# Kernel optimization log

Hardware: AMD Instinct MI355X
Metric: run time of the kernel (lower is better)

The kernel has to match this reference:

```python
import jax, jax.numpy as jnp
import numpy as np


def gcn_conv(x, src, dst, W, b, n_nodes):
    # PyG GCNConv default: add self-loops, symmetric normalization D^-1/2 A D^-1/2.
    h = x @ W  # [N, out]
    # degree with unit edge weights + self loop
    deg = jnp.zeros((n_nodes,), dtype=x.dtype).at[dst].add(1.0) + 1.0
    dinv = jax.lax.rsqrt(deg)  # deg >= 1, safe
    norm = dinv[src] * dinv[dst]  # [E]
    msg = h[src] * norm[:, None]  # [E, out] gather + scale
    out = jnp.zeros_like(h).at[dst].add(msg)  # scatter-add aggregate
    # self-loop contribution: norm_ii = dinv_i^2
    out = out + h * (dinv * dinv)[:, None]
    return out + b


def setup_inputs() -> dict:
    key = jax.random.key(0)
    ks = jax.random.split(key, 10)
    N, E, F_in, H, G = 100000, 1600000, 128, 128, 256
    x = jax.random.normal(ks[0], (N, F_in), dtype=jnp.float32)
    edge_index = jax.random.randint(ks[1], (2, E), 0, N, dtype=jnp.int64)
    batch = jnp.sort(jax.random.randint(ks[2], (N,), 0, G, dtype=jnp.int64))
    s1 = 1.0 / np.sqrt(F_in)
    s2 = 1.0 / np.sqrt(H)
    W1 = jax.random.uniform(ks[3], (F_in, H), jnp.float32, -s1, s1)
    b1 = jnp.zeros((H,), jnp.float32)
    W2 = jax.random.uniform(ks[4], (H, H), jnp.float32, -s2, s2)
    b2 = jnp.zeros((H,), jnp.float32)
    Wlin = jax.random.uniform(ks[5], (H, 2), jnp.float32, -s2, s2)
    blin = jax.random.uniform(ks[6], (2,), jnp.float32, -s2, s2)
    return {"x": x, "edge_index": edge_index, "batch": batch, "num_graphs": G,
            "W1": W1, "b1": b1, "W2": W2, "b2": b2, "Wlin": Wlin, "blin": blin}


def reference(x, edge_index, batch, num_graphs, W1, b1, W2, b2, Wlin, blin):
    n_nodes = x.shape[0]
    src, dst = edge_index[0], edge_index[1]
    h = jax.nn.relu(gcn_conv(x, src, dst, W1, b1, n_nodes))
    h = jax.nn.relu(gcn_conv(h, src, dst, W2, b2, n_nodes))
    # global_mean_pool over graphs
    sums = jax.ops.segment_sum(h, batch, num_segments=num_graphs)
    counts = jax.ops.segment_sum(jnp.ones((n_nodes,), h.dtype), batch, num_segments=num_graphs)
    pooled = sums / jnp.maximum(counts, 1.0)[:, None]  # [G, H]
    return pooled @ Wlin + blin  # [G, 2]
```

## Files before the change

### kernel.cpp

```cpp
#include <hip/hip_runtime.h>
#include <hip/hip_bf16.h>


#define FEAT 128
#define GRAPHS 256
#define CH 2048
#define BSH 8
#define MAXNB 512

typedef short bf16x8 __attribute__((ext_vector_type(8)));
typedef float f32x4 __attribute__((ext_vector_type(4)));

__device__ inline unsigned bf16rne(float f) {
    unsigned u = __float_as_uint(f);
    return (u + 0x7FFFu + ((u >> 16) & 1u)) >> 16;
}

#define SWZ(row, kbyte) ((kbyte) ^ (((row) & 7) << 4))

__global__ __launch_bounds__(256) void kb_hist(const int* __restrict__ dst, int E, int NB,
                                               int* __restrict__ bhist) {
    __shared__ int h[MAXNB];
    for (int i = threadIdx.x; i < NB; i += 256) h[i] = 0;
    __syncthreads();
    int stride = gridDim.x * 256;
    for (int i = blockIdx.x * 256 + threadIdx.x; i < E; i += stride)
        atomicAdd(&h[dst[i] >> BSH], 1);
    __syncthreads();
    for (int i = threadIdx.x; i < NB; i += 256)
        if (h[i]) atomicAdd(&bhist[i], h[i]);
}

__global__ void kb_scan(const int* __restrict__ bhist, int NB,
                        int* __restrict__ bbase, int* __restrict__ bcur) {
    __shared__ int s[512];
    int t = threadIdx.x;
    int v = (t < NB) ? bhist[t] : 0;
    s[t] = v;
    __syncthreads();
    for (int d = 1; d < 512; d <<= 1) {
        int a = (t >= d) ? s[t - d] : 0;
        __syncthreads();
        s[t] += a;
        __syncthreads();
    }
    if (t < NB) { int e = s[t] - v; bbase[t] = e; bcur[t] = e; }
}

__global__ __launch_bounds__(256) void kb_group(const int* __restrict__ src,
                                                const int* __restrict__ dst, int E, int NB,
                                                int* __restrict__ bcur,
                                                unsigned* __restrict__ stg) {
    __shared__ int lhist[MAXNB], lcur[MAXNB], gdelta[MAXNB], sc[512];
    __shared__ unsigned lpak[CH];
    __shared__ int gp[CH];
    int t = threadIdx.x;
    int base = blockIdx.x * CH;
    int n = E - base; if (n > CH) n = CH;

    for (int i = t; i < NB; i += 256) lhist[i] = 0;
    __syncthreads();

    unsigned pk[8]; int bk[8]; int nl = 0;
#pragma unroll
    for (int j = 0; j < 8; ++j) {
        int k = j * 256 + t;
        if (k < n) {
            int d = dst[base + k];
            int sv = src[base + k];
            int b = d >> BSH;
            pk[nl] = ((unsigned)(d & ((1 << BSH) - 1)) << 17) | (unsigned)sv;
            bk[nl] = b; nl++;
            atomicAdd(&lhist[b], 1);
        }
    }
    __syncthreads();

    for (int i = t; i < 512; i += 256) sc[i] = (i < NB) ? lhist[i] : 0;
    __syncthreads();
    for (int d = 1; d < 512; d <<= 1) {
        int a0 = (t >= d) ? sc[t - d] : 0;
        int a1 = sc[t + 256 - d];
        __syncthreads();
        sc[t] += a0; sc[t + 256] += a1;
        __syncthreads();
    }
    for (int i = t; i < NB; i += 256) {
        int c = lhist[i];
        int lb = sc[i] - c;
        lcur[i] = lb;
        int g = c ? atomicAdd(&bcur[i], c) : 0;
        gdelta[i] = g - lb;
    }
    __syncthreads();

    for (int j = 0; j < nl; ++j) {
        int b = bk[j];
        int slot = atomicAdd(&lcur[b], 1);
        lpak[slot] = pk[j];
        gp[slot] = gdelta[b] + slot;
    }
    __syncthreads();
    for (int i = t; i < n; i += 256) stg[gp[i]] = lpak[i];
}

__global__ __launch_bounds__(256) void kb_csr(const unsigned* __restrict__ stg,
                                              const int* __restrict__ bbase,
                                              const int* __restrict__ bhist, int N,
                                              int* __restrict__ ssrc, int* __restrict__ off,
                                              int* __restrict__ cnt, float* __restrict__ dinv) {
    __shared__ int h[256], lcur[256], sc[256];
    int b = blockIdx.x;
    int t = threadIdx.x;
    int s0 = bbase[b], m = bhist[b];
    h[t] = 0;
    __syncthreads();
    for (int i = t; i < m; i += 256) atomicAdd(&h[stg[s0 + i] >> 17], 1);
    __syncthreads();
    int v = h[t];
    sc[t] = v;
    __syncthreads();
    for (int d = 1; d < 256; d <<= 1) {
        int a = (t >= d) ? sc[t - d] : 0;
        __syncthreads();
        sc[t] += a;
        __syncthreads();
    }
    int lb = sc[t] - v;
    lcur[t] = lb;
    int node = (b << BSH) + t;
    if (node < N) {
        off[node] = s0 + lb;
        cnt[node] = v;
        dinv[node] = rsqrtf(1.0f + (float)v);
    }
    __syncthreads();
    for (int i = t; i < m; i += 256) {
        unsigned p = stg[s0 + i];
        int d = p >> 17;
        int r = atomicAdd(&lcur[d], 1);
        ssrc[s0 + r] = (int)(p & 0x1FFFFu);
    }
}

__global__ void k_gstart(const int* __restrict__ batch, int N, int G, int* __restrict__ gstart) {
    int i = blockIdx.x * blockDim.x + threadIdx.x;
    if (i >= N) return;
    int b = batch[i];
    int bp = (i == 0) ? -1 : batch[i - 1];
    for (int g = bp + 1; g <= b; ++g) gstart[g] = i;
    if (i == N - 1) {
        for (int g = b + 1; g <= G; ++g) gstart[g] = N;
    }
}

__global__ void k_wpre(const float* __restrict__ W, unsigned short* __restrict__ Wpre) {
    int tid = blockIdx.x * 256 + threadIdx.x;
    int frag = tid >> 6;
    int l = tid & 63;
    int cf = frag >> 2, ks = frag & 3;
    int col = cf * 16 + (l & 15);
    int k0 = ks * 32 + (l >> 4) * 8;
    unsigned short o[8];
#pragma unroll
    for (int j = 0; j < 8; ++j)
        o[j] = (unsigned short)bf16rne(W[(k0 + j) * 128 + col]);
    *(uint4*)(Wpre + (size_t)tid * 8) = *(const uint4*)o;
}

template <bool BF16IN>
__global__ __launch_bounds__(256, 4) void k_gemm_mfma(const void* __restrict__ Xv,
                                                      const unsigned short* __restrict__ Wpre,
                                                      const float* __restrict__ dinv,
                                                      unsigned short* __restrict__ HSB, int N) {
    __shared__ __align__(16) unsigned short sA[128 * 128];
    int t = threadIdx.x;
    int r0 = blockIdx.x * 128;
    int rows = N - r0; if (rows > 128) rows = 128;

    if constexpr (!BF16IN) {
        const float4* X4 = (const float4*)((const float*)Xv + (size_t)r0 * 128);
#pragma unroll
        for (int j = 0; j < 16; ++j) {
            int f = j * 256 + t;
            int row = f >> 5, q = f & 31;
            float4 v = make_float4(0.f, 0.f, 0.f, 0.f);
            if (row < rows) v = X4[f];
            unsigned lo = bf16rne(v.x) | (bf16rne(v.y) << 16);
            unsigned hi = bf16rne(v.z) | (bf16rne(v.w) << 16);
            int byte = row * 256 + SWZ(row, q * 8);
            *(uint2*)((char*)sA + byte) = make_uint2(lo, hi);
        }
    } else {
        const uint4* X4 = (const uint4*)((const unsigned short*)Xv + (size_t)r0 * 128);
#pragma unroll
        for (int j = 0; j < 8; ++j) {
            int f = j * 256 + t;
            int row = f >> 4, q = f & 15;
            uint4 v = make_uint4(0u, 0u, 0u, 0u);
            if (row < rows) v = X4[f];
            int byte = row * 256 + SWZ(row, q * 16);
            *(uint4*)((char*)sA + byte) = v;
        }
    }
    __syncthreads();

    int w = t >> 6, l = t & 63;
    int wr = (w >> 1) * 64, wc = (w & 1) * 64;
    int lr = l & 15, kc = l >> 4;

    f32x4 acc[4][4] = {};
    for (int ks = 0; ks < 4; ++ks) {
        bf16x8 a[4], b[4];
#pragma unroll
        for (int m = 0; m < 4; ++m) {
            int row = wr + m * 16 + lr;
            int byte = row * 256 + SWZ(row, ks * 64 + kc * 16);
            a[m] = *(const bf16x8*)((const char*)sA + byte);
        }
#pragma unroll
        for (int n = 0; n < 4; ++n) {
            int cf = (wc >> 4) + n;
            b[n] = *(const bf16x8*)(Wpre + ((size_t)((cf * 4 + ks) * 64 + l) * 8));
        }
#pragma unroll
        for (int m = 0; m < 4; ++m)
#pragma unroll
            for (int n = 0; n < 4; ++n)
                acc[m][n] = __builtin_amdgcn_mfma_f32_16x16x32_bf16(a[m], b[n], acc[m][n], 0, 0, 0);
    }
    __syncthreads();

#pragma unroll
    for (int m = 0; m < 4; ++m) {
        int rbase = wr + m * 16 + kc * 4;
#pragma unroll
        for (int r = 0; r < 4; ++r) {
            int row = rbase + r;
            float dv = (r0 + row < N) ? dinv[r0 + row] : 0.f;
#pragma unroll
            for (int n = 0; n < 4; ++n) {
                int col = wc + n * 16 + lr;
                sA[row * 128 + col] = (unsigned short)bf16rne(acc[m][n][r] * dv);
            }
        }
    }
    __syncthreads();
    uint4* dst4 = (uint4*)(HSB + (size_t)r0 * 128);
    const uint4* s4 = (const uint4*)sA;
#pragma unroll
    for (int j = 0; j < 8; ++j) {
        int f = j * 256 + t;
        int row = f >> 4;
        if (row < rows) dst4[f] = s4[f];
    }
}

#define GATHER1(uu)  { acc.x += __uint_as_float((uu) << 16); acc.y += __uint_as_float((uu) & 0xFFFF0000u); }
__global__ __launch_bounds__(256) void k_agg(const unsigned short* __restrict__ HSB,
                                             const int* __restrict__ off,
                                             const int* __restrict__ cnt,
                                             const int* __restrict__ ssrc,
                                             const float* __restrict__ dinv,
                                             const float* __restrict__ b,
                                             unsigned* __restrict__ OUTB, int N) {
    int wid = (blockIdx.x * blockDim.x + threadIdx.x) >> 6;
    int l = threadIdx.x & 63;
    if (wid >= N) return;
    int v = wid;
    const unsigned* T = (const unsigned*)HSB;
    unsigned su = T[(size_t)v * 64 + l];
    float2 acc;
    acc.x = __uint_as_float(su << 16);
    acc.y = __uint_as_float(su & 0xFFFF0000u);
    int s = off[v], e = s + cnt[v];
    int i = s;
    int head = (4 - (s & 3)) & 3;
    if (head > e - s) head = e - s;
    for (int k = 0; k < head; ++k, ++i) {
        unsigned u = T[(size_t)ssrc[i] * 64 + l];
        GATHER1(u)
    }
    for (; i + 8 <= e; i += 8) {
        int4 sa = *(const int4*)(ssrc + i);
        int4 sb = *(const int4*)(ssrc + i + 4);
        unsigned u0 = T[(size_t)sa.x * 64 + l];
        unsigned u1 = T[(size_t)sa.y * 64 + l];
        unsigned u2 = T[(size_t)sa.z * 64 + l];
        unsigned u3 = T[(size_t)sa.w * 64 + l];
        unsigned u4 = T[(size_t)sb.x * 64 + l];
        unsigned u5 = T[(size_t)sb.y * 64 + l];
        unsigned u6 = T[(size_t)sb.z * 64 + l];
        unsigned u7 = T[(size_t)sb.w * 64 + l];
        GATHER1(u0) GATHER1(u1) GATHER1(u2) GATHER1(u3)
        GATHER1(u4) GATHER1(u5) GATHER1(u6) GATHER1(u7)
    }
    if (i + 4 <= e) {
        int4 sa = *(const int4*)(ssrc + i);
        unsigned u0 = T[(size_t)sa.x * 64 + l];
        unsigned u1 = T[(size_t)sa.y * 64 + l];
        unsigned u2 = T[(size_t)sa.z * 64 + l];
        unsigned u3 = T[(size_t)sa.w * 64 + l];
        GATHER1(u0) GATHER1(u1) GATHER1(u2) GATHER1(u3)
        i += 4;
    }
    for (; i < e; ++i) {
        unsigned u = T[(size_t)ssrc[i] * 64 + l];
        GATHER1(u)
    }
    float dv = dinv[v];
    float2 bb = ((const float2*)b)[l];
    float ox = fmaxf(acc.x * dv + bb.x, 0.0f);
    float oy = fmaxf(acc.y * dv + bb.y, 0.0f);
    OUTB[(size_t)v * 64 + l] = bf16rne(ox) | (bf16rne(oy) << 16);
}

__global__ __launch_bounds__(256) void k_pool_head(const unsigned* __restrict__ H2,
                                                   const int* __restrict__ gstart,
                                                   const float* __restrict__ Wlin,
                                                   const float* __restrict__ blin,
                                                   float* __restrict__ out, int G) {
    __shared__ float2 stmp[256];
    __shared__ float sp[128];
    int g = blockIdx.x;
    int t = threadIdx.x;
    int p = t & 63, quarter = t >> 6;
    int s = gstart[g], e = gstart[g + 1];
    float2 acc = make_float2(0.f, 0.f);
    for (int i = s + quarter; i < e; i += 4) {
        unsigned u = H2[(size_t)i * 64 + p];
        acc.x += __uint_as_float(u << 16);
        acc.y += __uint_as_float(u & 0xFFFF0000u);
    }
    stmp[t] = acc;
    __syncthreads();
    if (t < 64) {
        float2 a = stmp[t];
        a.x += stmp[t + 64].x + stmp[t + 128].x + stmp[t + 192].x;
        a.y += stmp[t + 64].y + stmp[t + 128].y + stmp[t + 192].y;
        float inv = 1.0f / fmaxf((float)(e - s), 1.0f);
        sp[2 * t] = a.x * inv;
        sp[2 * t + 1] = a.y * inv;
    }
    __syncthreads();
    if (t < 2) {
        float a = 0.0f;
        for (int j = 0; j < 128; ++j) a += sp[j] * Wlin[j * 2 + t];
        out[g * 2 + t] = a + blin[t];
    }
}

extern "C" void kernel_launch(void* const* d_in, const int* in_sizes, int n_in,
                              void* d_out, int out_size, void* d_ws, size_t ws_size,
                              hipStream_t stream) {
    const float* x     = (const float*)d_in[0];
    const int*   ei    = (const int*)d_in[1];
    const int*   batch = (const int*)d_in[2];
    const float* W1    = (const float*)d_in[4];
    const float* b1    = (const float*)d_in[5];
    const float* W2    = (const float*)d_in[6];
    const float* b2    = (const float*)d_in[7];
    const float* Wlin  = (const float*)d_in[8];
    const float* blin  = (const float*)d_in[9];
    float* out = (float*)d_out;

    const int N = in_sizes[0] / FEAT;
    const int E = in_sizes[1] / 2;
    const int G = GRAPHS;
    const int NB = (N + (1 << BSH) - 1) >> BSH;
    const int* src = ei;
    const int* dst = ei + E;

    char* ws = (char*)d_ws;
    unsigned short* hsb = (unsigned short*)ws;
    unsigned short* hact = hsb + (size_t)N * FEAT;
    int*   ssrc = (int*)(hact + (size_t)N * FEAT);
    unsigned* stg = (unsigned*)(ssrc + E);
    int*   off  = (int*)(stg + E);
    int*   cnt  = off + N;
    float* dinv = (float*)(cnt + N);
    int*   bhist = (int*)(dinv + N);
    int*   bbase = bhist + MAXNB;
    int*   bcur  = bbase + MAXNB;
    int*   gstart = bcur + MAXNB;
    unsigned short* wpre1 = (unsigned short*)(gstart + G + 2);
    unsigned short* wpre2 = wpre1 + 16384;

    const int nb = (N + 255) / 256;
    const int nch = (E + CH - 1) / CH;
    const int ngb = (N + 127) / 128;

    hipMemsetAsync(bhist, 0, (size_t)NB * sizeof(int), stream);

    k_wpre<<<8, 256, 0, stream>>>(W1, wpre1);
    k_wpre<<<8, 256, 0, stream>>>(W2, wpre2);

    kb_hist<<<256, 256, 0, stream>>>(dst, E, NB, bhist);
    kb_scan<<<1, 512, 0, stream>>>(bhist, NB, bbase, bcur);
    kb_group<<<nch, 256, 0, stream>>>(src, dst, E, NB, bcur, stg);
    kb_csr<<<NB, 256, 0, stream>>>(stg, bbase, bhist, N, ssrc, off, cnt, dinv);

    k_gstart<<<nb, 256, 0, stream>>>(batch, N, G, gstart);

    k_gemm_mfma<false><<<ngb, 256, 0, stream>>>(x, wpre1, dinv, hsb, N);
    k_agg<<<(N + 3) / 4, 256, 0, stream>>>(hsb, off, cnt, ssrc, dinv, b1, (unsigned*)hact, N);
    k_gemm_mfma<true><<<ngb, 256, 0, stream>>>(hact, wpre2, dinv, hsb, N);
    k_agg<<<(N + 3) / 4, 256, 0, stream>>>(hsb, off, cnt, ssrc, dinv, b2, (unsigned*)hact, N);

    k_pool_head<<<G, 256, 0, stream>>>((const unsigned*)hact, gstart, Wlin, blin, out, G);
}
```

Measured before the change: 377.5 us.

## Quantize GEMM output to per-row int8 and gather int8 in aggregation

The GEMM epilogue now computes a per-row absmax scale and writes the scaled features as offset-by-128 int8 with a float scale per row, instead of bf16. The aggregation kernel gathers 4 bytes per lane, splits each node's edge list between two half-waves, dequantizes using the row scales, and combines the halves with a shuffle. This halves the bytes of the gather-bound aggregation, in exchange for int8 quantization error beyond the bf16 path and extra scale loads per edge.

```diff
diff --git a/kernel.cpp b/kernel.cpp
--- a/kernel.cpp
+++ b/kernel.cpp
@@ -168,12 +168,31 @@
     *(uint4*)(Wpre + (size_t)tid * 8) = *(const uint4*)o;
 }
 
+__device__ inline unsigned umax16pair(unsigned d, unsigned cur) {
+    unsigned a = d & 0x7FFF7FFFu;
+    unsigned lo = a & 0xFFFFu, hi = a >> 16;
+    unsigned m = lo > hi ? lo : hi;
+    return m > cur ? m : cur;
+}
+__device__ inline unsigned q8b(float x, float si) {
+    return (unsigned)(__float2int_rn(x * si) + 128) & 0xFFu;
+}
+__device__ inline unsigned pack2(unsigned d0, unsigned d1, float si) {
+    float x0 = __uint_as_float(d0 << 16);
+    float x1 = __uint_as_float(d0 & 0xFFFF0000u);
+    float x2 = __uint_as_float(d1 << 16);
+    float x3 = __uint_as_float(d1 & 0xFFFF0000u);
+    return q8b(x0, si) | (q8b(x1, si) << 8) | (q8b(x2, si) << 16) | (q8b(x3, si) << 24);
+}
+
 template <bool BF16IN>
 __global__ __launch_bounds__(256, 4) void k_gemm_mfma(const void* __restrict__ Xv,
                                                       const unsigned short* __restrict__ Wpre,
                                                       const float* __restrict__ dinv,
-                                                      unsigned short* __restrict__ HSB, int N) {
+                                                      unsigned char* __restrict__ Q8,
+                                                      float* __restrict__ srow, int N) {
     __shared__ __align__(16) unsigned short sA[128 * 128];
+    __shared__ unsigned sMaxH[256];
     int t = threadIdx.x;
     int r0 = blockIdx.x * 128;
     int rows = N - r0; if (rows > 128) rows = 128;
@@ -246,73 +265,115 @@
         }
     }
     __syncthreads();
-    uint4* dst4 = (uint4*)(HSB + (size_t)r0 * 128);
-    const uint4* s4 = (const uint4*)sA;
-#pragma unroll
-    for (int j = 0; j < 8; ++j) {
-        int f = j * 256 + t;
-        int row = f >> 4;
-        if (row < rows) dst4[f] = s4[f];
-    }
-}
-
-#define GATHER1(uu)  { acc.x += __uint_as_float((uu) << 16); acc.y += __uint_as_float((uu) & 0xFFFF0000u); }
-__global__ __launch_bounds__(256) void k_agg(const unsigned short* __restrict__ HSB,
-                                             const int* __restrict__ off,
-                                             const int* __restrict__ cnt,
-                                             const int* __restrict__ ssrc,
-                                             const float* __restrict__ dinv,
-                                             const float* __restrict__ b,
-                                             unsigned* __restrict__ OUTB, int N) {
+
+    {
+        int r = t >> 1, hh = t & 1;
+        const uint4* rowp = (const uint4*)(sA + r * 128 + hh * 64);
+        uint4 wreg[8];
+#pragma unroll
+        for (int j = 0; j < 8; ++j) wreg[j] = rowp[j];
+        unsigned mb = 0;
+#pragma unroll
+        for (int j = 0; j < 8; ++j) {
+            mb = umax16pair(wreg[j].x, mb);
+            mb = umax16pair(wreg[j].y, mb);
+            mb = umax16pair(wreg[j].z, mb);
+            mb = umax16pair(wreg[j].w, mb);
+        }
+        sMaxH[r * 2 + hh] = mb;
+        __syncthreads();
+        unsigned m0 = sMaxH[r * 2], m1 = sMaxH[r * 2 + 1];
+        unsigned m16 = m0 > m1 ? m0 : m1;
+        float mv = __uint_as_float(m16 << 16);
+        float si = (mv > 0.f) ? 127.0f / mv : 0.0f;
+        if (hh == 0 && r0 + r < N) srow[r0 + r] = mv * (1.0f / 127.0f);
+        if (r0 + r < N) {
+            unsigned q[16];
+#pragma unroll
+            for (int j = 0; j < 8; ++j) {
+                q[2 * j]     = pack2(wreg[j].x, wreg[j].y, si);
+                q[2 * j + 1] = pack2(wreg[j].z, wreg[j].w, si);
+            }
+            uint4* qo = (uint4*)(Q8 + (size_t)(r0 + r) * 128 + hh * 64);
+            qo[0] = make_uint4(q[0], q[1], q[2], q[3]);
+            qo[1] = make_uint4(q[4], q[5], q[6], q[7]);
+            qo[2] = make_uint4(q[8], q[9], q[10], q[11]);
+            qo[3] = make_uint4(q[12], q[13], q[14], q[15]);
+        }
+    }
+}
+
+#define ACC8(d, sc) { float _s = (sc);                       \
+    a0 += _s * (float)((d) & 0xFFu);                         \
+    a1 += _s * (float)(((d) >> 8) & 0xFFu);                  \
+    a2 += _s * (float)(((d) >> 16) & 0xFFu);                 \
+    a3 += _s * (float)((d) >> 24);                           \
+    ssum += _s; }
+
+__global__ __launch_bounds__(256) void k_agg8(const unsigned char* __restrict__ Q8,
+                                              const float* __restrict__ srow,
+                                              const int* __restrict__ off,
+                                              const int* __restrict__ cnt,
+                                              const int* __restrict__ ssrc,
+                                              const float* __restrict__ dinv,
+                                              const float* __restrict__ b,
+                                              unsigned* __restrict__ OUTB, int N) {
     int wid = (blockIdx.x * blockDim.x + threadIdx.x) >> 6;
+    if (wid >= N) return;
     int l = threadIdx.x & 63;
-    if (wid >= N) return;
+    int half = l >> 5, c4 = l & 31;
     int v = wid;
-    const unsigned* T = (const unsigned*)HSB;
-    unsigned su = T[(size_t)v * 64 + l];
-    float2 acc;
-    acc.x = __uint_as_float(su << 16);
-    acc.y = __uint_as_float(su & 0xFFFF0000u);
-    int s = off[v], e = s + cnt[v];
-    int i = s;
-    int head = (4 - (s & 3)) & 3;
-    if (head > e - s) head = e - s;
-    for (int k = 0; k < head; ++k, ++i) {
-        unsigned u = T[(size_t)ssrc[i] * 64 + l];
-        GATHER1(u)
-    }
-    for (; i + 8 <= e; i += 8) {
-        int4 sa = *(const int4*)(ssrc + i);
-        int4 sb = *(const int4*)(ssrc + i + 4);
-        unsigned u0 = T[(size_t)sa.x * 64 + l];
-        unsigned u1 = T[(size_t)sa.y * 64 + l];
-        unsigned u2 = T[(size_t)sa.z * 64 + l];
-        unsigned u3 = T[(size_t)sa.w * 64 + l];
-        unsigned u4 = T[(size_t)sb.x * 64 + l];
-        unsigned u5 = T[(size_t)sb.y * 64 + l];
-        unsigned u6 = T[(size_t)sb.z * 64 + l];
-        unsigned u7 = T[(size_t)sb.w * 64 + l];
-        GATHER1(u0) GATHER1(u1) GATHER1(u2) GATHER1(u3)
-        GATHER1(u4) GATHER1(u5) GATHER1(u6) GATHER1(u7)
-    }
-    if (i + 4 <= e) {
-        int4 sa = *(const int4*)(ssrc + i);
-        unsigned u0 = T[(size_t)sa.x * 64 + l];
-        unsigned u1 = T[(size_t)sa.y * 64 + l];
-        unsigned u2 = T[(size_t)sa.z * 64 + l];
-        unsigned u3 = T[(size_t)sa.w * 64 + l];
-        GATHER1(u0) GATHER1(u1) GATHER1(u2) GATHER1(u3)
-        i += 4;
-    }
-    for (; i < e; ++i) {
-        unsigned u = T[(size_t)ssrc[i] * 64 + l];
-        GATHER1(u)
-    }
-    float dv = dinv[v];
-    float2 bb = ((const float2*)b)[l];
-    float ox = fmaxf(acc.x * dv + bb.x, 0.0f);
-    float oy = fmaxf(acc.y * dv + bb.y, 0.0f);
-    OUTB[(size_t)v * 64 + l] = bf16rne(ox) | (bf16rne(oy) << 16);
+    int s = off[v], c = cnt[v];
+    int K = (c + 1) >> 1;
+    int ib = s + (half ? K : 0);
+    int ie = half ? (s + c) : (s + K);
+
+    float a0 = 0.f, a1 = 0.f, a2 = 0.f, a3 = 0.f, ssum = 0.f;
+    if (!half) {
+        unsigned d = *(const unsigned*)(Q8 + (size_t)v * 128 + c4 * 4);
+        float sc = srow[v];
+        ACC8(d, sc)
+    }
+    while (ib + 8 <= ie) {
+        int u0 = ssrc[ib],     u1 = ssrc[ib + 1], u2 = ssrc[ib + 2], u3 = ssrc[ib + 3];
+        int u4 = ssrc[ib + 4], u5 = ssrc[ib + 5], u6 = ssrc[ib + 6], u7 = ssrc[ib + 7];
+        unsigned d0 = *(const unsigned*)(Q8 + (size_t)u0 * 128 + c4 * 4);
+        unsigned d1 = *(const unsigned*)(Q8 + (size_t)u1 * 128 + c4 * 4);
+        unsigned d2 = *(const unsigned*)(Q8 + (size_t)u2 * 128 + c4 * 4);
+        unsigned d3 = *(const unsigned*)(Q8 + (size_t)u3 * 128 + c4 * 4);
+        unsigned d4 = *(const unsigned*)(Q8 + (size_t)u4 * 128 + c4 * 4);
+        unsigned d5 = *(const unsigned*)(Q8 + (size_t)u5 * 128 + c4 * 4);
+        unsigned d6 = *(const unsigned*)(Q8 + (size_t)u6 * 128 + c4 * 4);
+        unsigned d7 = *(const unsigned*)(Q8 + (size_t)u7 * 128 + c4 * 4);
+        float s0 = srow[u0], s1 = srow[u1], s2 = srow[u2], s3 = srow[u3];
+        float s4 = srow[u4], s5 = srow[u5], s6 = srow[u6], s7 = srow[u7];
+        ACC8(d0, s0) ACC8(d1, s1) ACC8(d2, s2) ACC8(d3, s3)
+        ACC8(d4, s4) ACC8(d5, s5) ACC8(d6, s6) ACC8(d7, s7)
+        ib += 8;
+    }
+    while (ib < ie) {
+        int u = ssrc[ib++];
+        unsigned d = *(const unsigned*)(Q8 + (size_t)u * 128 + c4 * 4);
+        float sc = srow[u];
+        ACC8(d, sc)
+    }
+    a0 += __shfl_xor(a0, 32);
+    a1 += __shfl_xor(a1, 32);
+    a2 += __shfl_xor(a2, 32);
+    a3 += __shfl_xor(a3, 32);
+    ssum += __shfl_xor(ssum, 32);
+    if (!half) {
+        float dv = dinv[v];
+        float4 bb = *(const float4*)(b + c4 * 4);
+        float o0 = fmaxf((a0 - 128.f * ssum) * dv + bb.x, 0.f);
+        float o1 = fmaxf((a1 - 128.f * ssum) * dv + bb.y, 0.f);
+        float o2 = fmaxf((a2 - 128.f * ssum) * dv + bb.z, 0.f);
+        float o3 = fmaxf((a3 - 128.f * ssum) * dv + bb.w, 0.f);
+        uint2 wv;
+        wv.x = bf16rne(o0) | (bf16rne(o1) << 16);
+        wv.y = bf16rne(o2) | (bf16rne(o3) << 16);
+        ((uint2*)(OUTB + (size_t)v * 64))[c4] = wv;
+    }
 }
 
 __global__ __launch_bounds__(256) void k_pool_head(const unsigned* __restrict__ H2,
@@ -372,8 +433,9 @@
     const int* dst = ei + E;
 
     char* ws = (char*)d_ws;
-    unsigned short* hsb = (unsigned short*)ws;
-    unsigned short* hact = hsb + (size_t)N * FEAT;
+    unsigned char* q8 = (unsigned char*)ws;
+    float* srow = (float*)(q8 + (size_t)N * FEAT);
+    unsigned short* hact = (unsigned short*)(srow + N);
     int*   ssrc = (int*)(hact + (size_t)N * FEAT);
     unsigned* stg = (unsigned*)(ssrc + E);
     int*   off  = (int*)(stg + E);
@@ -402,10 +464,10 @@
 
     k_gstart<<<nb, 256, 0, stream>>>(batch, N, G, gstart);
 
-    k_gemm_mfma<false><<<ngb, 256, 0, stream>>>(x, wpre1, dinv, hsb, N);
-    k_agg<<<(N + 3) / 4, 256, 0, stream>>>(hsb, off, cnt, ssrc, dinv, b1, (unsigned*)hact, N);
-    k_gemm_mfma<true><<<ngb, 256, 0, stream>>>(hact, wpre2, dinv, hsb, N);
-    k_agg<<<(N + 3) / 4, 256, 0, stream>>>(hsb, off, cnt, ssrc, dinv, b2, (unsigned*)hact, N);
+    k_gemm_mfma<false><<<ngb, 256, 0, stream>>>(x, wpre1, dinv, q8, srow, N);
+    k_agg8<<<(N + 3) / 4, 256, 0, stream>>>(q8, srow, off, cnt, ssrc, dinv, b1, (unsigned*)hact, N);
+    k_gemm_mfma<true><<<ngb, 256, 0, stream>>>(hact, wpre2, dinv, q8, srow, N);
+    k_agg8<<<(N + 3) / 4, 256, 0, stream>>>(q8, srow, off, cnt, ssrc, dinv, b2, (unsigned*)hact, N);
 
     k_pool_head<<<G, 256, 0, stream>>>((const unsigned*)hact, gstart, Wlin, blin, out, G);
 }
```

New measurement: 383.5 us. Within noise of the previous version (+1.6%).
